# Kernel optimization log

Hardware: AMD Instinct MI355X
Metric: run time of the kernel (lower is better)

## Reference

```python
import jax, jax.numpy as jnp
import numpy as np

B, CIN, COUT, H, W = 8, 128, 128, 64, 64
KH = KW = 3
STRIDE = PAD = 1
DIL = 1
K = KH * KW
EPS = 1e-4


def setup_inputs() -> dict:
    key = jax.random.key(0)
    k1, k2, k3 = jax.random.split(key, 3)
    Ho = (H + 2 * PAD - DIL * (KH - 1) - 1) // STRIDE + 1
    Wo = (W + 2 * PAD - DIL * (KW - 1) - 1) // STRIDE + 1
    x = jax.random.normal(k1, (B, CIN, H, W), dtype=jnp.float32)
    offset = jax.random.normal(k2, (B, 2 * K, Ho, Wo), dtype=jnp.float32)
    weight = jax.random.normal(k3, (COUT, CIN, KH, KW), dtype=jnp.float32) * 0.05
    return {"x": x, "offset": offset, "weight": weight}


def _bilinear_gather(x, py, px):
    # x: [B, C, H, W]; py/px: [B, K, Ho, Wo] float sampling positions
    Bn, C, Hn, Wn = x.shape
    x_flat = x.reshape(Bn, C, Hn * Wn)
    y0 = jnp.floor(py)
    x0 = jnp.floor(px)
    ly = py - y0  # fractional parts
    lx = px - x0
    out = 0.0
    corners = [(0.0, 0.0, (1 - ly) * (1 - lx)), (0.0, 1.0, (1 - ly) * lx),
               (1.0, 0.0, ly * (1 - lx)), (1.0, 1.0, ly * lx)]
    for dy, dx, wgt in corners:
        yy = y0 + dy
        xx = x0 + dx
        valid = (yy >= 0) & (yy < Hn) & (xx >= 0) & (xx < Wn)
        yi = jnp.clip(yy, 0, Hn - 1).astype(jnp.int32)
        xi = jnp.clip(xx, 0, Wn - 1).astype(jnp.int32)
        idx = (yi * Wn + xi).reshape(Bn, -1)  # [B, K*Ho*Wo]
        g = jax.vmap(lambda xf, ib: jnp.take(xf, ib, axis=1))(x_flat, idx)  # [B, C, N]
        out = out + g * (wgt * valid.astype(x.dtype)).reshape(Bn, 1, -1)
    return out  # [B, C, K*Ho*Wo]


def reference(x, offset, weight) -> jnp.ndarray:
    Bn = x.shape[0]
    Ho, Wo = offset.shape[2], offset.shape[3]
    # --- weight normalization (per output channel, per kernel tap) ---
    norm_fac = (KH * KW) ** 0.5
    length = jnp.sqrt(jnp.sum(jnp.square(weight) + EPS, axis=1, keepdims=True))  # [O,1,kh,kw]
    wn = weight / length / norm_fac  # [O, Cin, kh, kw]
    # --- sampling positions ---
    off = offset.reshape(Bn, K, 2, Ho, Wo)
    off_y, off_x = off[:, :, 0], off[:, :, 1]
    ky, kx = jnp.meshgrid(jnp.arange(KH), jnp.arange(KW), indexing="ij")
    ky = (ky.reshape(K) * DIL).astype(jnp.float32)
    kx = (kx.reshape(K) * DIL).astype(jnp.float32)
    base_y = (jnp.arange(Ho) * STRIDE - PAD).astype(jnp.float32)
    base_x = (jnp.arange(Wo) * STRIDE - PAD).astype(jnp.float32)
    py = base_y[None, None, :, None] + ky[None, :, None, None] + off_y  # [B,K,Ho,Wo]
    px = base_x[None, None, None, :] + kx[None, :, None, None] + off_x
    # --- deformable im2col + GEMM ---
    cols = _bilinear_gather(x, py, px).reshape(Bn, CIN, K, Ho, Wo)
    out = jnp.einsum("bckhw,ock->bohw", cols, wn.reshape(COUT, CIN, K))
    return out
```

## Files before the change

### kernel.cpp

```cpp
#include <hip/hip_runtime.h>
#include <math.h>


typedef __attribute__((ext_vector_type(8))) short short8;
typedef __attribute__((ext_vector_type(4))) float floatx4;

static __device__ __forceinline__ unsigned int f2bf(float f) {
    unsigned int u = __float_as_uint(f);
    u += 0x7fffu + ((u >> 16) & 1u);
    return u >> 16;
}
static __device__ __forceinline__ float bflo(unsigned int w) {
    return __uint_as_float(w << 16);
}
static __device__ __forceinline__ float bfhi(unsigned int w) {
    return __uint_as_float(w & 0xffff0000u);
}

__global__ void prep_k(const float* __restrict__ x, const float* __restrict__ w,
                       unsigned int* __restrict__ xt32, unsigned short* __restrict__ wb) {
    __shared__ float lds[128 * 65];
    const int tid = threadIdx.x;

    if (blockIdx.x < 512) {
        const int b = blockIdx.x >> 6, h = blockIdx.x & 63;
        const float* xp = x + (b * 128 * 64 + h) * 64;
        #pragma unroll 4
        for (int i = 0; i < 32; i++) {
            const int c = i * 4 + (tid >> 6);
            const int ww = tid & 63;
            lds[c * 65 + ww] = xp[c * 4096 + ww];
        }
        __syncthreads();
        unsigned int* xo = xt32 + blockIdx.x * 4096;
        #pragma unroll 4
        for (int i = 0; i < 16; i++) {
            const int flat2 = i * 256 + tid;
            const int ww = flat2 >> 6, cp = flat2 & 63;
            const unsigned int lo = f2bf(lds[(2 * cp) * 65 + ww]);
            const unsigned int hi = f2bf(lds[(2 * cp + 1) * 65 + ww]);
            xo[flat2] = lo | (hi << 16);
        }
    } else {
        const int o = (blockIdx.x - 512) * 4 + (tid >> 6);
        const int lane = tid & 63;
        const float* wo = w + o * 1152;
        float v[18];
        #pragma unroll
        for (int i = 0; i < 18; i++) v[i] = wo[lane * 18 + i];
        float s[9];
        #pragma unroll
        for (int k = 0; k < 9; k++) s[k] = v[k] * v[k] + v[9 + k] * v[9 + k];
        #pragma unroll
        for (int d = 32; d >= 1; d >>= 1) {
            #pragma unroll
            for (int k = 0; k < 9; k++) s[k] += __shfl_xor(s[k], d, 64);
        }
        const int c0 = 2 * lane, c1 = c0 + 1;
        #pragma unroll
        for (int k = 0; k < 9; k++) {
            const float inv = 1.0f / (3.0f * sqrtf(s[k] + 0.0128f));
            wb[((k * 16 + (c0 >> 3)) * 128 + o) * 8 + (c0 & 7)] = (unsigned short)f2bf(v[k] * inv);
            wb[((k * 16 + (c1 >> 3)) * 128 + o) * 8 + (c1 & 7)] = (unsigned short)f2bf(v[9 + k] * inv);
        }
    }
}

static __device__ __forceinline__ uint4 combine4(const float4 wvv,
                                                 const uint4 r0, const uint4 r1,
                                                 const uint4 r2, const uint4 r3) {
    uint4 pk;
    {
        const float lo = wvv.x*bflo(r0.x) + wvv.y*bflo(r1.x) + wvv.z*bflo(r2.x) + wvv.w*bflo(r3.x);
        const float hi = wvv.x*bfhi(r0.x) + wvv.y*bfhi(r1.x) + wvv.z*bfhi(r2.x) + wvv.w*bfhi(r3.x);
        pk.x = f2bf(lo) | (f2bf(hi) << 16);
    }
    {
        const float lo = wvv.x*bflo(r0.y) + wvv.y*bflo(r1.y) + wvv.z*bflo(r2.y) + wvv.w*bflo(r3.y);
        const float hi = wvv.x*bfhi(r0.y) + wvv.y*bfhi(r1.y) + wvv.z*bfhi(r2.y) + wvv.w*bfhi(r3.y);
        pk.y = f2bf(lo) | (f2bf(hi) << 16);
    }
    {
        const float lo = wvv.x*bflo(r0.z) + wvv.y*bflo(r1.z) + wvv.z*bflo(r2.z) + wvv.w*bflo(r3.z);
        const float hi = wvv.x*bfhi(r0.z) + wvv.y*bfhi(r1.z) + wvv.z*bfhi(r2.z) + wvv.w*bfhi(r3.z);
        pk.z = f2bf(lo) | (f2bf(hi) << 16);
    }
    {
        const float lo = wvv.x*bflo(r0.w) + wvv.y*bflo(r1.w) + wvv.z*bflo(r2.w) + wvv.w*bflo(r3.w);
        const float hi = wvv.x*bfhi(r0.w) + wvv.y*bfhi(r1.w) + wvv.z*bfhi(r2.w) + wvv.w*bfhi(r3.w);
        pk.w = f2bf(lo) | (f2bf(hi) << 16);
    }
    return pk;
}

__global__ __launch_bounds__(256, 4) void dconv_k(
    const unsigned short* __restrict__ xt, const float* __restrict__ off,
    const unsigned short* __restrict__ wb, float* __restrict__ out)
{
    __shared__ float4 tapw[288];
    __shared__ int4   tapi[288];
    __shared__ alignas(16) unsigned short colsS[2][16 * 264];

    const int idx = blockIdx.x;
    const int b = idx & 7;
    const int ho = (idx >> 3) & 63;
    const int pix0 = (idx >> 9) * 32;
    const int tid = threadIdx.x;

    for (int t = tid; t < 288; t += 256) {
        const int k = t >> 5, p = t & 31;
        const int pw = pix0 + p;
        const int oidx = ((b * 18 + 2 * k) * 64 + ho) * 64 + pw;
        const float offy = off[oidx];
        const float offx = off[oidx + 4096];
        const float py = (float)(ho - 1 + (k / 3)) + offy;
        const float px = (float)(pw - 1 + (k % 3)) + offx;
        const float y0f = floorf(py), x0f = floorf(px);
        const float ly = py - y0f, lx = px - x0f;
        const int y0 = (int)y0f, x0 = (int)x0f;
        const int y1 = y0 + 1, x1 = x0 + 1;
        const float vy0 = (y0 >= 0 && y0 < 64) ? 1.0f : 0.0f;
        const float vy1 = (y1 >= 0 && y1 < 64) ? 1.0f : 0.0f;
        const float vx0 = (x0 >= 0 && x0 < 64) ? 1.0f : 0.0f;
        const float vx1 = (x1 >= 0 && x1 < 64) ? 1.0f : 0.0f;
        const int yc0 = min(max(y0, 0), 63), yc1 = min(max(y1, 0), 63);
        const int xc0 = min(max(x0, 0), 63), xc1 = min(max(x1, 0), 63);
        tapw[t] = make_float4((1.0f - ly) * (1.0f - lx) * vy0 * vx0,
                              (1.0f - ly) * lx          * vy0 * vx1,
                              ly * (1.0f - lx)          * vy1 * vx0,
                              ly * lx                   * vy1 * vx1);
        tapi[t] = make_int4((yc0 * 64 + xc0) * 128, (yc0 * 64 + xc1) * 128,
                            (yc1 * 64 + xc0) * 128, (yc1 * 64 + xc1) * 128);
    }
    __syncthreads();

    const int lane = tid & 63, wv = tid >> 6;
    const int quad = lane >> 4, l16 = lane & 15;
    const int g = tid & 15, prow = tid >> 4;
    const unsigned short* xb = xt + b * (64 * 64 * 128);
    const int wbase = wv * 32;

    floatx4 acc0[2], acc1[2];
    #pragma unroll
    for (int t = 0; t < 2; t++) { acc0[t] = (floatx4)0.0f; acc1[t] = (floatx4)0.0f; }

    #pragma unroll
    for (int i = 0; i < 2; i++) {
        const int p = i * 16 + prow;
        const float4 wvv = tapw[p];
        const int4  iv  = tapi[p];
        const uint4 r0 = *(const uint4*)(xb + iv.x + g * 8);
        const uint4 r1 = *(const uint4*)(xb + iv.y + g * 8);
        const uint4 r2 = *(const uint4*)(xb + iv.z + g * 8);
        const uint4 r3 = *(const uint4*)(xb + iv.w + g * 8);
        *(uint4*)&colsS[0][g * 264 + p * 8] = combine4(wvv, r0, r1, r2, r3);
    }
    __syncthreads();

    for (int k = 0; k < 9; k++) {
        const int cur = k & 1;

        const unsigned short* wk = wb + k * 16384;
        short8 a0[4], a1[4];
        #pragma unroll
        for (int q = 0; q < 4; q++) {
            const int cgrp = q * 4 + quad;
            a0[q] = *(const short8*)(wk + (cgrp * 128 + wbase + l16) * 8);
            a1[q] = *(const short8*)(wk + (cgrp * 128 + wbase + 16 + l16) * 8);
        }

        uint4 r[2][4];
        if (k < 8) {
            #pragma unroll
            for (int i = 0; i < 2; i++) {
                const int p = i * 16 + prow;
                const int4 iv = tapi[(k + 1) * 32 + p];
                r[i][0] = *(const uint4*)(xb + iv.x + g * 8);
                r[i][1] = *(const uint4*)(xb + iv.y + g * 8);
                r[i][2] = *(const uint4*)(xb + iv.z + g * 8);
                r[i][3] = *(const uint4*)(xb + iv.w + g * 8);
            }
        }

        #pragma unroll
        for (int q = 0; q < 4; q++) {
            const int cgrp = q * 4 + quad;
            #pragma unroll
            for (int t = 0; t < 2; t++) {
                const short8 bf = *(const short8*)&colsS[cur][cgrp * 264 + (t * 16 + l16) * 8];
                acc0[t] = __builtin_amdgcn_mfma_f32_16x16x32_bf16(a0[q], bf, acc0[t], 0, 0, 0);
                acc1[t] = __builtin_amdgcn_mfma_f32_16x16x32_bf16(a1[q], bf, acc1[t], 0, 0, 0);
            }
        }

        if (k < 8) {
            #pragma unroll
            for (int i = 0; i < 2; i++) {
                const int p = i * 16 + prow;
                const float4 wvv = tapw[(k + 1) * 32 + p];
                *(uint4*)&colsS[cur ^ 1][g * 264 + p * 8] =
                    combine4(wvv, r[i][0], r[i][1], r[i][2], r[i][3]);
            }
            __syncthreads();
        }
    }

    float* ob = out + b * 128 * 4096 + ho * 64 + pix0;
    #pragma unroll
    for (int t = 0; t < 2; t++) {
        const int pix = t * 16 + l16;
        #pragma unroll
        for (int r2 = 0; r2 < 4; r2++) {
            ob[(wbase + quad * 4 + r2) * 4096 + pix]      = acc0[t][r2];
            ob[(wbase + 16 + quad * 4 + r2) * 4096 + pix] = acc1[t][r2];
        }
    }
}

extern "C" void kernel_launch(void* const* d_in, const int* in_sizes, int n_in,
                              void* d_out, int out_size, void* d_ws, size_t ws_size,
                              hipStream_t stream) {
    const float* x   = (const float*)d_in[0];
    const float* off = (const float*)d_in[1];
    const float* w   = (const float*)d_in[2];
    float* out = (float*)d_out;

    unsigned short* xt = (unsigned short*)d_ws;
    unsigned short* wbuf = xt + 8 * 64 * 64 * 128;

    hipLaunchKernelGGL(prep_k,  dim3(544),  dim3(256), 0, stream,
                       x, w, (unsigned int*)xt, wbuf);
    hipLaunchKernelGGL(dconv_k, dim3(1024), dim3(256), 0, stream, xt, off, wbuf, out);
}
```

Before: 99.96 us.

## Gather all nine taps into LDS upfront, then run MFMA loop unsynchronized

Replaces the double-buffered per-tap gather/MFMA pipeline with a single phase that gathers all nine taps' bilinear columns into a 9-slot LDS buffer, followed by one barrier and a barrier-free MFMA loop. Tap metadata is compressed into a packed uint2 holding fp16 fractional weights and biased 8-bit integer corners, with validity and clamping recomputed per use. LDS use grows to about 76 KB per block and launch bounds drop to 2 blocks per SM, trading occupancy and gather/MFMA overlap for fewer barriers. The fp16 fractions and 8-bit coordinate packing add slight precision and range risk (offsets beyond about ±32 would wrap).

After: 105.7 us. 5.7% more time.

```diff
diff --git a/kernel.cpp b/kernel.cpp
--- a/kernel.cpp
+++ b/kernel.cpp
@@ -1,4 +1,5 @@
 #include <hip/hip_runtime.h>
+#include <hip/hip_fp16.h>
 #include <math.h>
 
 
@@ -66,40 +67,40 @@
     }
 }
 
-static __device__ __forceinline__ uint4 combine4(const float4 wvv,
+static __device__ __forceinline__ uint4 combine4(const float w0, const float w1,
+                                                 const float w2, const float w3,
                                                  const uint4 r0, const uint4 r1,
                                                  const uint4 r2, const uint4 r3) {
     uint4 pk;
     {
-        const float lo = wvv.x*bflo(r0.x) + wvv.y*bflo(r1.x) + wvv.z*bflo(r2.x) + wvv.w*bflo(r3.x);
-        const float hi = wvv.x*bfhi(r0.x) + wvv.y*bfhi(r1.x) + wvv.z*bfhi(r2.x) + wvv.w*bfhi(r3.x);
+        const float lo = w0*bflo(r0.x) + w1*bflo(r1.x) + w2*bflo(r2.x) + w3*bflo(r3.x);
+        const float hi = w0*bfhi(r0.x) + w1*bfhi(r1.x) + w2*bfhi(r2.x) + w3*bfhi(r3.x);
         pk.x = f2bf(lo) | (f2bf(hi) << 16);
     }
     {
-        const float lo = wvv.x*bflo(r0.y) + wvv.y*bflo(r1.y) + wvv.z*bflo(r2.y) + wvv.w*bflo(r3.y);
-        const float hi = wvv.x*bfhi(r0.y) + wvv.y*bfhi(r1.y) + wvv.z*bfhi(r2.y) + wvv.w*bfhi(r3.y);
+        const float lo = w0*bflo(r0.y) + w1*bflo(r1.y) + w2*bflo(r2.y) + w3*bflo(r3.y);
+        const float hi = w0*bfhi(r0.y) + w1*bfhi(r1.y) + w2*bfhi(r2.y) + w3*bfhi(r3.y);
         pk.y = f2bf(lo) | (f2bf(hi) << 16);
     }
     {
-        const float lo = wvv.x*bflo(r0.z) + wvv.y*bflo(r1.z) + wvv.z*bflo(r2.z) + wvv.w*bflo(r3.z);
-        const float hi = wvv.x*bfhi(r0.z) + wvv.y*bfhi(r1.z) + wvv.z*bfhi(r2.z) + wvv.w*bfhi(r3.z);
+        const float lo = w0*bflo(r0.z) + w1*bflo(r1.z) + w2*bflo(r2.z) + w3*bflo(r3.z);
+        const float hi = w0*bfhi(r0.z) + w1*bfhi(r1.z) + w2*bfhi(r2.z) + w3*bfhi(r3.z);
         pk.z = f2bf(lo) | (f2bf(hi) << 16);
     }
     {
-        const float lo = wvv.x*bflo(r0.w) + wvv.y*bflo(r1.w) + wvv.z*bflo(r2.w) + wvv.w*bflo(r3.w);
-        const float hi = wvv.x*bfhi(r0.w) + wvv.y*bfhi(r1.w) + wvv.z*bfhi(r2.w) + wvv.w*bfhi(r3.w);
+        const float lo = w0*bflo(r0.w) + w1*bflo(r1.w) + w2*bflo(r2.w) + w3*bflo(r3.w);
+        const float hi = w0*bfhi(r0.w) + w1*bfhi(r1.w) + w2*bfhi(r2.w) + w3*bfhi(r3.w);
         pk.w = f2bf(lo) | (f2bf(hi) << 16);
     }
     return pk;
 }
 
-__global__ __launch_bounds__(256, 4) void dconv_k(
+__global__ __launch_bounds__(256, 2) void dconv_k(
     const unsigned short* __restrict__ xt, const float* __restrict__ off,
     const unsigned short* __restrict__ wb, float* __restrict__ out)
 {
-    __shared__ float4 tapw[288];
-    __shared__ int4   tapi[288];
-    __shared__ alignas(16) unsigned short colsS[2][16 * 264];
+    __shared__ uint2 tapP[288];
+    __shared__ alignas(16) unsigned short colsS[9][16 * 264];
 
     const int idx = blockIdx.x;
     const int b = idx & 7;
@@ -117,20 +118,13 @@
         const float px = (float)(pw - 1 + (k % 3)) + offx;
         const float y0f = floorf(py), x0f = floorf(px);
         const float ly = py - y0f, lx = px - x0f;
-        const int y0 = (int)y0f, x0 = (int)x0f;
-        const int y1 = y0 + 1, x1 = x0 + 1;
-        const float vy0 = (y0 >= 0 && y0 < 64) ? 1.0f : 0.0f;
-        const float vy1 = (y1 >= 0 && y1 < 64) ? 1.0f : 0.0f;
-        const float vx0 = (x0 >= 0 && x0 < 64) ? 1.0f : 0.0f;
-        const float vx1 = (x1 >= 0 && x1 < 64) ? 1.0f : 0.0f;
-        const int yc0 = min(max(y0, 0), 63), yc1 = min(max(y1, 0), 63);
-        const int xc0 = min(max(x0, 0), 63), xc1 = min(max(x1, 0), 63);
-        tapw[t] = make_float4((1.0f - ly) * (1.0f - lx) * vy0 * vx0,
-                              (1.0f - ly) * lx          * vy0 * vx1,
-                              ly * (1.0f - lx)          * vy1 * vx0,
-                              ly * lx                   * vy1 * vx1);
-        tapi[t] = make_int4((yc0 * 64 + xc0) * 128, (yc0 * 64 + xc1) * 128,
-                            (yc1 * 64 + xc0) * 128, (yc1 * 64 + xc1) * 128);
+        const unsigned int lyh = __half_as_ushort(__float2half_rn(ly));
+        const unsigned int lxh = __half_as_ushort(__float2half_rn(lx));
+        const int y0b = (int)y0f + 32, x0b = (int)x0f + 32;
+        uint2 pk;
+        pk.x = lyh | (lxh << 16);
+        pk.y = (unsigned int)(y0b & 0xFF) | ((unsigned int)(x0b & 0xFF) << 8);
+        tapP[t] = pk;
     }
     __syncthreads();
 
@@ -140,68 +134,49 @@
     const unsigned short* xb = xt + b * (64 * 64 * 128);
     const int wbase = wv * 32;
 
+    for (int k = 0; k < 9; k++) {
+        #pragma unroll
+        for (int i = 0; i < 2; i++) {
+            const int p = i * 16 + prow;
+            const uint2 tp = tapP[k * 32 + p];
+            const float ly = __half2float(__ushort_as_half((unsigned short)(tp.x & 0xffff)));
+            const float lx = __half2float(__ushort_as_half((unsigned short)(tp.x >> 16)));
+            const int y0 = (int)(tp.y & 0xFF) - 32;
+            const int x0 = (int)((tp.y >> 8) & 0xFF) - 32;
+            const int y1 = y0 + 1, x1 = x0 + 1;
+            const float fy0 = (y0 >= 0 && y0 < 64) ? (1.0f - ly) : 0.0f;
+            const float fy1 = (y1 >= 0 && y1 < 64) ? ly : 0.0f;
+            const float fx0 = (x0 >= 0 && x0 < 64) ? (1.0f - lx) : 0.0f;
+            const float fx1 = (x1 >= 0 && x1 < 64) ? lx : 0.0f;
+            const int yc0 = min(max(y0, 0), 63), yc1 = min(max(y1, 0), 63);
+            const int xc0 = min(max(x0, 0), 63), xc1 = min(max(x1, 0), 63);
+            const uint4 r0 = *(const uint4*)(xb + ((yc0 * 64 + xc0) << 7) + g * 8);
+            const uint4 r1 = *(const uint4*)(xb + ((yc0 * 64 + xc1) << 7) + g * 8);
+            const uint4 r2 = *(const uint4*)(xb + ((yc1 * 64 + xc0) << 7) + g * 8);
+            const uint4 r3 = *(const uint4*)(xb + ((yc1 * 64 + xc1) << 7) + g * 8);
+            *(uint4*)&colsS[k][g * 264 + p * 8] =
+                combine4(fy0 * fx0, fy0 * fx1, fy1 * fx0, fy1 * fx1, r0, r1, r2, r3);
+        }
+    }
+    __syncthreads();
+
     floatx4 acc0[2], acc1[2];
     #pragma unroll
     for (int t = 0; t < 2; t++) { acc0[t] = (floatx4)0.0f; acc1[t] = (floatx4)0.0f; }
 
-    #pragma unroll
-    for (int i = 0; i < 2; i++) {
-        const int p = i * 16 + prow;
-        const float4 wvv = tapw[p];
-        const int4  iv  = tapi[p];
-        const uint4 r0 = *(const uint4*)(xb + iv.x + g * 8);
-        const uint4 r1 = *(const uint4*)(xb + iv.y + g * 8);
-        const uint4 r2 = *(const uint4*)(xb + iv.z + g * 8);
-        const uint4 r3 = *(const uint4*)(xb + iv.w + g * 8);
-        *(uint4*)&colsS[0][g * 264 + p * 8] = combine4(wvv, r0, r1, r2, r3);
-    }
-    __syncthreads();
-
     for (int k = 0; k < 9; k++) {
-        const int cur = k & 1;
-
         const unsigned short* wk = wb + k * 16384;
-        short8 a0[4], a1[4];
         #pragma unroll
         for (int q = 0; q < 4; q++) {
             const int cgrp = q * 4 + quad;
-            a0[q] = *(const short8*)(wk + (cgrp * 128 + wbase + l16) * 8);
-            a1[q] = *(const short8*)(wk + (cgrp * 128 + wbase + 16 + l16) * 8);
-        }
-
-        uint4 r[2][4];
-        if (k < 8) {
-            #pragma unroll
-            for (int i = 0; i < 2; i++) {
-                const int p = i * 16 + prow;
-                const int4 iv = tapi[(k + 1) * 32 + p];
-                r[i][0] = *(const uint4*)(xb + iv.x + g * 8);
-                r[i][1] = *(const uint4*)(xb + iv.y + g * 8);
-                r[i][2] = *(const uint4*)(xb + iv.z + g * 8);
-                r[i][3] = *(const uint4*)(xb + iv.w + g * 8);
-            }
-        }
-
-        #pragma unroll
-        for (int q = 0; q < 4; q++) {
-            const int cgrp = q * 4 + quad;
+            const short8 a0 = *(const short8*)(wk + (cgrp * 128 + wbase + l16) * 8);
+            const short8 a1 = *(const short8*)(wk + (cgrp * 128 + wbase + 16 + l16) * 8);
             #pragma unroll
             for (int t = 0; t < 2; t++) {
-                const short8 bf = *(const short8*)&colsS[cur][cgrp * 264 + (t * 16 + l16) * 8];
-                acc0[t] = __builtin_amdgcn_mfma_f32_16x16x32_bf16(a0[q], bf, acc0[t], 0, 0, 0);
-                acc1[t] = __builtin_amdgcn_mfma_f32_16x16x32_bf16(a1[q], bf, acc1[t], 0, 0, 0);
+                const short8 bf = *(const short8*)&colsS[k][cgrp * 264 + (t * 16 + l16) * 8];
+                acc0[t] = __builtin_amdgcn_mfma_f32_16x16x32_bf16(a0, bf, acc0[t], 0, 0, 0);
+                acc1[t] = __builtin_amdgcn_mfma_f32_16x16x32_bf16(a1, bf, acc1[t], 0, 0, 0);
             }
-        }
-
-        if (k < 8) {
-            #pragma unroll
-            for (int i = 0; i < 2; i++) {
-                const int p = i * 16 + prow;
-                const float4 wvv = tapw[(k + 1) * 32 + p];
-                *(uint4*)&colsS[cur ^ 1][g * 264 + p * 8] =
-                    combine4(wvv, r[i][0], r[i][1], r[i][2], r[i][3]);
-            }
-            __syncthreads();
         }
     }
 
```
